# Optimization experiments

Hardware: AMD Instinct MI355X
Metric: run time of the kernel (lower is better)

## Reference

```python
import jax, jax.numpy as jnp
import numpy as np

B, T, D = 2048, 100, 128
HID = [512, 256, 128]
ALPHA, NOISE_STD = 0.2, 0.05


def _lin_init(key, fan_in, fan_out):
    k1, k2 = jax.random.split(key)
    b = 1.0 / np.sqrt(fan_in)
    W = jax.random.uniform(k1, (fan_in, fan_out), minval=-b, maxval=b, dtype=jnp.float32)
    bias = jax.random.uniform(k2, (fan_out,), minval=-b, maxval=b, dtype=jnp.float32)
    return W, bias


def setup_inputs() -> dict:
    key = jax.random.key(0)
    ks = jax.random.split(key, 10)
    x = jax.random.normal(ks[0], (B, T, D), dtype=jnp.float32)
    noise = jax.random.normal(ks[1], (B, T - 1, HID[-1]), dtype=jnp.float32)
    e_w0, e_b0 = _lin_init(ks[2], D, HID[0])
    e_w1, e_b1 = _lin_init(ks[3], HID[0], HID[1])
    e_w2, e_b2 = _lin_init(ks[4], HID[1], HID[2])
    d_w0, d_b0 = _lin_init(ks[5], HID[2], HID[1])
    d_w1, d_b1 = _lin_init(ks[6], HID[1], HID[0])
    d_w2, d_b2 = _lin_init(ks[7], HID[0], D)
    m = jax.random.normal(ks[8], (HID[-1], 2), dtype=jnp.float32)
    n = jax.random.normal(ks[9], (HID[-1], 2), dtype=jnp.float32)
    return {"x": x, "noise": noise, "seq_len": T,
            "e_w0": e_w0, "e_b0": e_b0, "e_w1": e_w1, "e_b1": e_b1,
            "e_w2": e_w2, "e_b2": e_b2, "d_w0": d_w0, "d_b0": d_b0,
            "d_w1": d_w1, "d_b1": d_b1, "d_w2": d_w2, "d_b2": d_b2,
            "m": m, "n": n}


def reference(x, noise, seq_len, e_w0, e_b0, e_w1, e_b1, e_w2, e_b2,
              d_w0, d_b0, d_w1, d_b1, d_w2, d_b2, m, n):
    hs = m.shape[0]  # latent size (128)
    x = jnp.where(jnp.isnan(x), 0.0, x)  # NaN masking as in Autoencoder.forward

    def encoder(v):
        v = jax.nn.relu(v @ e_w0 + e_b0)
        v = jax.nn.relu(v @ e_w1 + e_b1)
        return v @ e_w2 + e_b2

    def decoder(v):
        v = jax.nn.relu(v @ d_w0 + d_b0)
        v = jax.nn.relu(v @ d_w1 + d_b1)
        return v @ d_w2 + d_b2

    h_enc = encoder(x)              # (B, T, hs)
    x_reconstruct = decoder(h_enc)  # (B, T, D)
    h0 = h_enc[:, 0, :]             # (B, hs)
    x0 = x[:, 0, :]                 # (B, D)

    def step(h, nz):
        r = jnp.tanh(h)
        # low-rank recurrence: rank-2 update m n^T / hidden_size
        dh = ALPHA * (-h + (r @ n) @ m.T / hs) + NOISE_STD * nz
        h = h + dh
        out = decoder(jnp.tanh(h))
        return h, (h, out)

    _, (zs, outs) = jax.lax.scan(step, h0, jnp.swapaxes(noise, 0, 1))
    z_pred = jnp.concatenate([h0[:, None, :], jnp.swapaxes(zs, 0, 1)], axis=1)
    x_pred = jnp.concatenate([x0[:, None, :], jnp.swapaxes(outs, 0, 1)], axis=1)
    return x_pred, x_reconstruct, z_pred
```

## Files before the change

kernel.cpp:

```cpp
#include <hip/hip_runtime.h>
#include <math.h>

namespace {

constexpr int B_  = 2048;
constexpr int T_  = 100;
constexpr int D_  = 128;
constexpr int BT_ = B_ * T_;
constexpr int M_  = 64;

using f32x4  = __attribute__((ext_vector_type(4))) float;
using bf16x8 = __attribute__((ext_vector_type(8))) __bf16;

enum { MODE_ENC = 0, MODE_ID = 1, MODE_TANH = 2 };

__device__ __forceinline__ unsigned short f2bf(float f) {
  unsigned int u = __float_as_uint(f);
  return (unsigned short)((u + 0x7FFFu + ((u >> 16) & 1u)) >> 16);
}
__device__ __forceinline__ unsigned int pack2(float a, float b) {
  return (unsigned int)f2bf(a) | ((unsigned int)f2bf(b) << 16);
}
__device__ __forceinline__ float ftanh(float x) {
  const float e = __expf(2.0f * x);
  return 1.0f - 2.0f / (e + 1.0f);
}

template <int KGEMM, int NT, int KFW>
__device__ __forceinline__ void gemm(const char* __restrict__ A, const int astr,
                                     const unsigned short* __restrict__ Wt,
                                     f32x4 (&acc)[NT][4], const int lrow, const int lk) {
  constexpr int NK = KGEMM / 32;
  const int key = lrow << 4;
  const unsigned short* wl = Wt + lk * 8;
#pragma unroll
  for (int kk = 0; kk < NK; ++kk) {
    int4 breg[NT];
#pragma unroll
    for (int nt = 0; nt < NT; ++nt)
      breg[nt] = *reinterpret_cast<const int4*>(
          wl + (size_t)(nt * 16 + lrow) * KFW + kk * 32);
    bf16x8 act[4];
#pragma unroll
    for (int s = 0; s < 4; ++s)
      act[s] = __builtin_bit_cast(bf16x8,
          *reinterpret_cast<const int4*>(A + (s * 16 + lrow) * astr + ((kk * 64 + lk * 16) ^ key)));
#pragma unroll
    for (int nt = 0; nt < NT; ++nt) {
      const bf16x8 w = __builtin_bit_cast(bf16x8, breg[nt]);
#pragma unroll
      for (int s = 0; s < 4; ++s)
        acc[nt][s] = __builtin_amdgcn_mfma_f32_16x16x32_bf16(w, act[s], acc[nt][s], 0, 0, 0);
    }
  }
}

template <int NT>
__device__ __forceinline__ void init_bias(f32x4 (&acc)[NT][4], const float* __restrict__ bias,
                                          const int lk) {
#pragma unroll
  for (int nt = 0; nt < NT; ++nt) {
    const f32x4 bv = *reinterpret_cast<const f32x4*>(bias + nt * 16 + lk * 4);
#pragma unroll
    for (int s = 0; s < 4; ++s) acc[nt][s] = bv;
  }
}

template <int NT, bool RELU>
__device__ __forceinline__ void store_lds_pk(char* __restrict__ dst, const int strideB,
                                             const int colLocal0, f32x4 (&acc)[NT][4],
                                             const int lrow, const int lk) {
  const int key = lrow << 4;
#pragma unroll
  for (int nt = 0; nt < NT; ++nt) {
    const int colb = (colLocal0 + nt * 16 + lk * 4) * 2;
#pragma unroll
    for (int s = 0; s < 4; ++s) {
      float v0 = acc[nt][s][0], v1 = acc[nt][s][1], v2 = acc[nt][s][2], v3 = acc[nt][s][3];
      if (RELU) {
        v0 = fmaxf(v0, 0.f); v1 = fmaxf(v1, 0.f); v2 = fmaxf(v2, 0.f); v3 = fmaxf(v3, 0.f);
      }
      uint2 w;
      w.x = pack2(v0, v1);
      w.y = pack2(v2, v3);
      *reinterpret_cast<uint2*>(dst + (s * 16 + lrow) * strideB + (colb ^ key)) = w;
    }
  }
}

template <int MODE>
__device__ __forceinline__ int rowmap(const int rl) {
  if constexpr (MODE == MODE_TANH) {
    const int b = rl / 99;
    return b * T_ + (rl - b * 99) + 1;
  }
  return rl;
}

template <int MODE>
__device__ __forceinline__ void store_global(float* __restrict__ gout, f32x4 (&acc)[1][4],
                                             const int r0, const int col0,
                                             const int lrow, const int lk) {
#pragma unroll
  for (int s = 0; s < 4; ++s) {
    const int g = rowmap<MODE>(r0 + s * 16 + lrow);
    *reinterpret_cast<float4*>(gout + (size_t)g * D_ + col0 + lk * 4) =
        __builtin_bit_cast(float4, acc[0][s]);
  }
}

template <int MODE>
__device__ __forceinline__ void stage(const float* __restrict__ in, char* __restrict__ X,
                                      float* __restrict__ xpred0,
                                      const int r0, const int tid) {
#pragma unroll
  for (int i = 0; i < 2; ++i) {
    const int c   = tid + i * 512;
    const int row = c >> 4;
    const int cb  = c & 15;
    const int rl  = r0 + row;
    const int g   = rowmap<MODE>(rl);
    const float4* gp = reinterpret_cast<const float4*>(in + (size_t)g * D_ + cb * 8);
    float4 v0 = gp[0], v1 = gp[1];
    if constexpr (MODE == MODE_ENC) {
      v0.x = (v0.x == v0.x) ? v0.x : 0.f;  v0.y = (v0.y == v0.y) ? v0.y : 0.f;
      v0.z = (v0.z == v0.z) ? v0.z : 0.f;  v0.w = (v0.w == v0.w) ? v0.w : 0.f;
      v1.x = (v1.x == v1.x) ? v1.x : 0.f;  v1.y = (v1.y == v1.y) ? v1.y : 0.f;
      v1.z = (v1.z == v1.z) ? v1.z : 0.f;  v1.w = (v1.w == v1.w) ? v1.w : 0.f;
      if (rl % T_ == 0) {
        float4* xp = reinterpret_cast<float4*>(xpred0 + (size_t)g * D_ + cb * 8);
        xp[0] = v0; xp[1] = v1;
      }
    }
    if constexpr (MODE == MODE_TANH) {
      v0.x = ftanh(v0.x); v0.y = ftanh(v0.y); v0.z = ftanh(v0.z); v0.w = ftanh(v0.w);
      v1.x = ftanh(v1.x); v1.y = ftanh(v1.y); v1.z = ftanh(v1.z); v1.w = ftanh(v1.w);
    }
    int4 pk;
    pk.x = (int)pack2(v0.x, v0.y); pk.y = (int)pack2(v0.z, v0.w);
    pk.z = (int)pack2(v1.x, v1.y); pk.w = (int)pack2(v1.z, v1.w);
    *reinterpret_cast<int4*>(X + row * 256 + ((cb * 16) ^ ((row & 15) << 4))) = pk;
  }
}

template <int MODE>
__device__ __forceinline__ void dec_body(const unsigned short* __restrict__ dW0t, const float* __restrict__ d_b0,
                                         const unsigned short* __restrict__ dW1t, const float* __restrict__ d_b1,
                                         const unsigned short* __restrict__ dW2t, const float* __restrict__ d_b2,
                                         float* __restrict__ gout,
                                         char* __restrict__ X, char* __restrict__ Y,
                                         const int r0, const int wave, const int lrow, const int lk) {
  f32x4 acc1[2][4];
  init_bias<2>(acc1, d_b0 + wave * 32, lk);
  gemm<128, 2, 128>(X, 256, dW0t + (size_t)(wave * 32) * 128, acc1, lrow, lk);
  store_lds_pk<2, true>(Y, 512, wave * 32, acc1, lrow, lk);
  __syncthreads();

  f32x4 acc3[1][4];
  init_bias<1>(acc3, d_b2 + wave * 16, lk);
#pragma unroll
  for (int q = 0; q < 4; ++q) {
    f32x4 acc2[1][4];
    init_bias<1>(acc2, d_b1 + q * 128 + wave * 16, lk);
    gemm<256, 1, 256>(Y, 512, dW1t + (size_t)(q * 128 + wave * 16) * 256, acc2, lrow, lk);
    if (q) __syncthreads();
    store_lds_pk<1, true>(X, 256, wave * 16, acc2, lrow, lk);
    __syncthreads();
    gemm<128, 1, 512>(X, 256, dW2t + (size_t)(wave * 16) * 512 + q * 128, acc3, lrow, lk);
  }
  store_global<MODE>(gout, acc3, r0, wave * 16, lrow, lk);
}

__launch_bounds__(512, 4)
__global__ void enc_dec_kernel(const float* __restrict__ in,
                               const unsigned short* __restrict__ eW0t, const float* __restrict__ e_b0,
                               const unsigned short* __restrict__ eW1t, const float* __restrict__ e_b1,
                               const unsigned short* __restrict__ eW2t, const float* __restrict__ e_b2,
                               const unsigned short* __restrict__ dW0t, const float* __restrict__ d_b0,
                               const unsigned short* __restrict__ dW1t, const float* __restrict__ d_b1,
                               const unsigned short* __restrict__ dW2t, const float* __restrict__ d_b2,
                               float* __restrict__ z, float* __restrict__ x_rec,
                               float* __restrict__ x_pred) {
  __shared__ __align__(16) char X[M_ * 256];
  __shared__ __align__(16) char Y[M_ * 512];

  const int tid  = threadIdx.x;
  const int wave = tid >> 6;
  const int lane = tid & 63;
  const int lrow = lane & 15;
  const int lk   = lane >> 4;
  const int r0   = blockIdx.x * M_;

  stage<MODE_ENC>(in, X, x_pred, r0, tid);
  __syncthreads();

  f32x4 acc2[2][4];
  init_bias<2>(acc2, e_b1 + wave * 32, lk);
#pragma unroll
  for (int h = 0; h < 2; ++h) {
    f32x4 acc1[2][4];
    init_bias<2>(acc1, e_b0 + h * 256 + wave * 32, lk);
    gemm<128, 2, 128>(X, 256, eW0t + (size_t)(h * 256 + wave * 32) * 128, acc1, lrow, lk);
    if (h) __syncthreads();
    store_lds_pk<2, true>(Y, 512, wave * 32, acc1, lrow, lk);
    __syncthreads();
    gemm<256, 2, 512>(Y, 512, eW1t + (size_t)(wave * 32) * 512 + h * 256, acc2, lrow, lk);
  }
  __syncthreads();

  f32x4 acc3[1][4];
  init_bias<1>(acc3, e_b2 + wave * 16, lk);
#pragma unroll
  for (int hh = 0; hh < 2; ++hh) {
    if ((wave >> 2) == hh)
      store_lds_pk<2, true>(X, 256, (wave & 3) * 32, acc2, lrow, lk);
    __syncthreads();
    gemm<128, 1, 256>(X, 256, eW2t + (size_t)(wave * 16) * 256 + hh * 128, acc3, lrow, lk);
    __syncthreads();
  }
  store_lds_pk<1, false>(X, 256, wave * 16, acc3, lrow, lk);
  store_global<MODE_ENC>(z, acc3, r0, wave * 16, lrow, lk);
  __syncthreads();

  dec_body<MODE_ID>(dW0t, d_b0, dW1t, d_b1, dW2t, d_b2, x_rec, X, Y, r0, wave, lrow, lk);
}

__launch_bounds__(512, 4)
__global__ void pred_dec_kernel(const float* __restrict__ zin,
                                const unsigned short* __restrict__ dW0t, const float* __restrict__ d_b0,
                                const unsigned short* __restrict__ dW1t, const float* __restrict__ d_b1,
                                const unsigned short* __restrict__ dW2t, const float* __restrict__ d_b2,
                                float* __restrict__ x_pred) {
  __shared__ __align__(16) char X[M_ * 256];
  __shared__ __align__(16) char Y[M_ * 512];

  const int tid  = threadIdx.x;
  const int wave = tid >> 6;
  const int lane = tid & 63;
  const int lrow = lane & 15;
  const int lk   = lane >> 4;
  const int r0   = blockIdx.x * M_;

  stage<MODE_TANH>(zin, X, nullptr, r0, tid);
  __syncthreads();
  dec_body<MODE_TANH>(dW0t, d_b0, dW1t, d_b1, dW2t, d_b2, x_pred, X, Y, r0, wave, lrow, lk);
}

__global__ void wprep_all_kernel(const float* __restrict__ s0, const float* __restrict__ s1,
                                 const float* __restrict__ s2, const float* __restrict__ s3,
                                 const float* __restrict__ s4, const float* __restrict__ s5,
                                 unsigned short* __restrict__ d0, unsigned short* __restrict__ d1,
                                 unsigned short* __restrict__ d2, unsigned short* __restrict__ d3,
                                 unsigned short* __restrict__ d4, unsigned short* __restrict__ d5) {
  const int id = blockIdx.x * blockDim.x + threadIdx.x;
  const float* src; unsigned short* dst; int K, N, l;
  if (id < 65536)       { src = s0; dst = d0; K = 128; N = 512; l = id; }
  else if (id < 196608) { src = s1; dst = d1; K = 512; N = 256; l = id - 65536; }
  else if (id < 229376) { src = s2; dst = d2; K = 256; N = 128; l = id - 196608; }
  else if (id < 262144) { src = s3; dst = d3; K = 128; N = 256; l = id - 229376; }
  else if (id < 393216) { src = s4; dst = d4; K = 256; N = 512; l = id - 262144; }
  else                  { src = s5; dst = d5; K = 512; N = 128; l = id - 393216; }
  const int k = l / N;
  const int n = l - k * N;
  dst[(size_t)n * K + k] = f2bf(src[l]);
}

__global__ void rnn_scan_kernel(const float* __restrict__ noise,
                                const float* __restrict__ m, const float* __restrict__ n,
                                float* __restrict__ z) {
  const int gtid = blockIdx.x * blockDim.x + threadIdx.x;
  const int b = gtid >> 6;
  const int lane = threadIdx.x & 63;
  const int k0 = lane, k1 = lane + 64;

  const float mk00 = m[k0 * 2], mk01 = m[k0 * 2 + 1];
  const float mk10 = m[k1 * 2], mk11 = m[k1 * 2 + 1];
  const float nk00 = n[k0 * 2], nk01 = n[k0 * 2 + 1];
  const float nk10 = n[k1 * 2], nk11 = n[k1 * 2 + 1];

  float* zb = z + (size_t)b * T_ * D_;
  const float* nzb = noise + (size_t)b * (T_ - 1) * D_;
  float h0 = zb[k0];
  float h1 = zb[k1];

#pragma unroll 1
  for (int t = 0; t < T_ - 1; ++t) {
    const float r0v = tanhf(h0);
    const float r1v = tanhf(h1);
    float p0 = r0v * nk00 + r1v * nk10;
    float p1 = r0v * nk01 + r1v * nk11;
#pragma unroll
    for (int off = 32; off > 0; off >>= 1) {
      p0 += __shfl_xor(p0, off);
      p1 += __shfl_xor(p1, off);
    }
    const float v0 = (p0 * mk00 + p1 * mk01) * (1.0f / 128.0f);
    const float v1 = (p0 * mk10 + p1 * mk11) * (1.0f / 128.0f);
    const float nz0 = nzb[t * D_ + k0];
    const float nz1 = nzb[t * D_ + k1];
    h0 += 0.2f * (v0 - h0) + 0.05f * nz0;
    h1 += 0.2f * (v1 - h1) + 0.05f * nz1;
    zb[(t + 1) * D_ + k0] = h0;
    zb[(t + 1) * D_ + k1] = h1;
  }
}

}

extern "C" void kernel_launch(void* const* d_in, const int* in_sizes, int n_in,
                              void* d_out, int out_size, void* d_ws, size_t ws_size,
                              hipStream_t stream) {
  (void)in_sizes; (void)n_in; (void)ws_size; (void)out_size;

  const float* x     = (const float*)d_in[0];
  const float* noise = (const float*)d_in[1];
  const float* e_w0 = (const float*)d_in[3];
  const float* e_b0 = (const float*)d_in[4];
  const float* e_w1 = (const float*)d_in[5];
  const float* e_b1 = (const float*)d_in[6];
  const float* e_w2 = (const float*)d_in[7];
  const float* e_b2 = (const float*)d_in[8];
  const float* d_w0 = (const float*)d_in[9];
  const float* d_b0 = (const float*)d_in[10];
  const float* d_w1 = (const float*)d_in[11];
  const float* d_b1 = (const float*)d_in[12];
  const float* d_w2 = (const float*)d_in[13];
  const float* d_b2 = (const float*)d_in[14];
  const float* m    = (const float*)d_in[15];
  const float* n    = (const float*)d_in[16];

  float* out    = (float*)d_out;
  float* x_pred = out;
  float* x_rec  = out + (size_t)BT_ * D_;
  float* z      = out + 2 * (size_t)BT_ * D_;

  unsigned short* ws = (unsigned short*)d_ws;
  unsigned short* eW0t = ws;
  unsigned short* eW1t = ws + 65536;
  unsigned short* eW2t = ws + 196608;
  unsigned short* dW0t = ws + 229376;
  unsigned short* dW1t = ws + 262144;
  unsigned short* dW2t = ws + 393216;

  wprep_all_kernel<<<458752 / 256, 256, 0, stream>>>(e_w0, e_w1, e_w2, d_w0, d_w1, d_w2,
                                                     eW0t, eW1t, eW2t, dW0t, dW1t, dW2t);

  enc_dec_kernel<<<BT_ / M_, 512, 0, stream>>>(x,
      eW0t, e_b0, eW1t, e_b1, eW2t, e_b2,
      dW0t, d_b0, dW1t, d_b1, dW2t, d_b2,
      z, x_rec, x_pred);

  rnn_scan_kernel<<<B_ / 4, 256, 0, stream>>>(noise, m, n, z);

  pred_dec_kernel<<<(B_ * (T_ - 1)) / M_, 512, 0, stream>>>(z,
      dW0t, d_b0, dW1t, d_b1, dW2t, d_b2, x_pred);
}
```

Baseline: 664.5 us.

## Halve row tile to 32 and use 4-wave blocks with wider per-wave column tiles

```diff
diff --git a/kernel.cpp b/kernel.cpp
--- a/kernel.cpp
+++ b/kernel.cpp
@@ -7,7 +7,7 @@
 constexpr int T_  = 100;
 constexpr int D_  = 128;
 constexpr int BT_ = B_ * T_;
-constexpr int M_  = 64;
+constexpr int M_  = 32;
 
 using f32x4  = __attribute__((ext_vector_type(4))) float;
 using bf16x8 = __attribute__((ext_vector_type(8))) __bf16;
@@ -29,7 +29,7 @@
 template <int KGEMM, int NT, int KFW>
 __device__ __forceinline__ void gemm(const char* __restrict__ A, const int astr,
                                      const unsigned short* __restrict__ Wt,
-                                     f32x4 (&acc)[NT][4], const int lrow, const int lk) {
+                                     f32x4 (&acc)[NT][2], const int lrow, const int lk) {
   constexpr int NK = KGEMM / 32;
   const int key = lrow << 4;
   const unsigned short* wl = Wt + lk * 8;
@@ -40,42 +40,42 @@
     for (int nt = 0; nt < NT; ++nt)
       breg[nt] = *reinterpret_cast<const int4*>(
           wl + (size_t)(nt * 16 + lrow) * KFW + kk * 32);
-    bf16x8 act[4];
-#pragma unroll
-    for (int s = 0; s < 4; ++s)
+    bf16x8 act[2];
+#pragma unroll
+    for (int s = 0; s < 2; ++s)
       act[s] = __builtin_bit_cast(bf16x8,
           *reinterpret_cast<const int4*>(A + (s * 16 + lrow) * astr + ((kk * 64 + lk * 16) ^ key)));
 #pragma unroll
     for (int nt = 0; nt < NT; ++nt) {
       const bf16x8 w = __builtin_bit_cast(bf16x8, breg[nt]);
 #pragma unroll
-      for (int s = 0; s < 4; ++s)
+      for (int s = 0; s < 2; ++s)
         acc[nt][s] = __builtin_amdgcn_mfma_f32_16x16x32_bf16(w, act[s], acc[nt][s], 0, 0, 0);
     }
   }
 }
 
 template <int NT>
-__device__ __forceinline__ void init_bias(f32x4 (&acc)[NT][4], const float* __restrict__ bias,
+__device__ __forceinline__ void init_bias(f32x4 (&acc)[NT][2], const float* __restrict__ bias,
                                           const int lk) {
 #pragma unroll
   for (int nt = 0; nt < NT; ++nt) {
     const f32x4 bv = *reinterpret_cast<const f32x4*>(bias + nt * 16 + lk * 4);
 #pragma unroll
-    for (int s = 0; s < 4; ++s) acc[nt][s] = bv;
+    for (int s = 0; s < 2; ++s) acc[nt][s] = bv;
   }
 }
 
 template <int NT, bool RELU>
 __device__ __forceinline__ void store_lds_pk(char* __restrict__ dst, const int strideB,
-                                             const int colLocal0, f32x4 (&acc)[NT][4],
+                                             const int colLocal0, f32x4 (&acc)[NT][2],
                                              const int lrow, const int lk) {
   const int key = lrow << 4;
 #pragma unroll
   for (int nt = 0; nt < NT; ++nt) {
     const int colb = (colLocal0 + nt * 16 + lk * 4) * 2;
 #pragma unroll
-    for (int s = 0; s < 4; ++s) {
+    for (int s = 0; s < 2; ++s) {
       float v0 = acc[nt][s][0], v1 = acc[nt][s][1], v2 = acc[nt][s][2], v3 = acc[nt][s][3];
       if (RELU) {
         v0 = fmaxf(v0, 0.f); v1 = fmaxf(v1, 0.f); v2 = fmaxf(v2, 0.f); v3 = fmaxf(v3, 0.f);
@@ -97,15 +97,17 @@
   return rl;
 }
 
-template <int MODE>
-__device__ __forceinline__ void store_global(float* __restrict__ gout, f32x4 (&acc)[1][4],
+template <int MODE, int NT>
+__device__ __forceinline__ void store_global(float* __restrict__ gout, f32x4 (&acc)[NT][2],
                                              const int r0, const int col0,
                                              const int lrow, const int lk) {
 #pragma unroll
-  for (int s = 0; s < 4; ++s) {
+  for (int s = 0; s < 2; ++s) {
     const int g = rowmap<MODE>(r0 + s * 16 + lrow);
-    *reinterpret_cast<float4*>(gout + (size_t)g * D_ + col0 + lk * 4) =
-        __builtin_bit_cast(float4, acc[0][s]);
+    float* gr = gout + (size_t)g * D_ + col0 + lk * 4;
+#pragma unroll
+    for (int nt = 0; nt < NT; ++nt)
+      *reinterpret_cast<float4*>(gr + nt * 16) = __builtin_bit_cast(float4, acc[nt][s]);
   }
 }
 
@@ -115,7 +117,7 @@
                                       const int r0, const int tid) {
 #pragma unroll
   for (int i = 0; i < 2; ++i) {
-    const int c   = tid + i * 512;
+    const int c   = tid + i * 256;
     const int row = c >> 4;
     const int cb  = c & 15;
     const int rl  = r0 + row;
@@ -150,28 +152,31 @@
                                          float* __restrict__ gout,
                                          char* __restrict__ X, char* __restrict__ Y,
                                          const int r0, const int wave, const int lrow, const int lk) {
-  f32x4 acc1[2][4];
-  init_bias<2>(acc1, d_b0 + wave * 32, lk);
-  gemm<128, 2, 128>(X, 256, dW0t + (size_t)(wave * 32) * 128, acc1, lrow, lk);
-  store_lds_pk<2, true>(Y, 512, wave * 32, acc1, lrow, lk);
-  __syncthreads();
-
-  f32x4 acc3[1][4];
-  init_bias<1>(acc3, d_b2 + wave * 16, lk);
+#pragma unroll
+  for (int p = 0; p < 2; ++p) {
+    f32x4 acc1[2][2];
+    init_bias<2>(acc1, d_b0 + p * 128 + wave * 32, lk);
+    gemm<128, 2, 128>(X, 256, dW0t + (size_t)(p * 128 + wave * 32) * 128, acc1, lrow, lk);
+    store_lds_pk<2, true>(Y, 512, p * 128 + wave * 32, acc1, lrow, lk);
+  }
+  __syncthreads();
+
+  f32x4 acc3[2][2];
+  init_bias<2>(acc3, d_b2 + wave * 32, lk);
 #pragma unroll
   for (int q = 0; q < 4; ++q) {
-    f32x4 acc2[1][4];
-    init_bias<1>(acc2, d_b1 + q * 128 + wave * 16, lk);
-    gemm<256, 1, 256>(Y, 512, dW1t + (size_t)(q * 128 + wave * 16) * 256, acc2, lrow, lk);
+    f32x4 acc2[2][2];
+    init_bias<2>(acc2, d_b1 + q * 128 + wave * 32, lk);
+    gemm<256, 2, 256>(Y, 512, dW1t + (size_t)(q * 128 + wave * 32) * 256, acc2, lrow, lk);
     if (q) __syncthreads();
-    store_lds_pk<1, true>(X, 256, wave * 16, acc2, lrow, lk);
+    store_lds_pk<2, true>(X, 256, wave * 32, acc2, lrow, lk);
     __syncthreads();
-    gemm<128, 1, 512>(X, 256, dW2t + (size_t)(wave * 16) * 512 + q * 128, acc3, lrow, lk);
-  }
-  store_global<MODE>(gout, acc3, r0, wave * 16, lrow, lk);
-}
-
-__launch_bounds__(512, 4)
+    gemm<128, 2, 512>(X, 256, dW2t + (size_t)(wave * 32) * 512 + q * 128, acc3, lrow, lk);
+  }
+  store_global<MODE, 2>(gout, acc3, r0, wave * 32, lrow, lk);
+}
+
+__launch_bounds__(256, 4)
 __global__ void enc_dec_kernel(const float* __restrict__ in,
                                const unsigned short* __restrict__ eW0t, const float* __restrict__ e_b0,
                                const unsigned short* __restrict__ eW1t, const float* __restrict__ e_b1,
@@ -194,38 +199,44 @@
   stage<MODE_ENC>(in, X, x_pred, r0, tid);
   __syncthreads();
 
-  f32x4 acc2[2][4];
-  init_bias<2>(acc2, e_b1 + wave * 32, lk);
+  f32x4 acc2[2][2][2];
+#pragma unroll
+  for (int p2 = 0; p2 < 2; ++p2)
+    init_bias<2>(acc2[p2], e_b1 + p2 * 128 + wave * 32, lk);
 #pragma unroll
   for (int h = 0; h < 2; ++h) {
-    f32x4 acc1[2][4];
-    init_bias<2>(acc1, e_b0 + h * 256 + wave * 32, lk);
-    gemm<128, 2, 128>(X, 256, eW0t + (size_t)(h * 256 + wave * 32) * 128, acc1, lrow, lk);
     if (h) __syncthreads();
-    store_lds_pk<2, true>(Y, 512, wave * 32, acc1, lrow, lk);
+#pragma unroll
+    for (int p = 0; p < 2; ++p) {
+      f32x4 acc1[2][2];
+      init_bias<2>(acc1, e_b0 + h * 256 + p * 128 + wave * 32, lk);
+      gemm<128, 2, 128>(X, 256, eW0t + (size_t)(h * 256 + p * 128 + wave * 32) * 128, acc1, lrow, lk);
+      store_lds_pk<2, true>(Y, 512, p * 128 + wave * 32, acc1, lrow, lk);
+    }
     __syncthreads();
-    gemm<256, 2, 512>(Y, 512, eW1t + (size_t)(wave * 32) * 512 + h * 256, acc2, lrow, lk);
-  }
-  __syncthreads();
-
-  f32x4 acc3[1][4];
-  init_bias<1>(acc3, e_b2 + wave * 16, lk);
-#pragma unroll
-  for (int hh = 0; hh < 2; ++hh) {
-    if ((wave >> 2) == hh)
-      store_lds_pk<2, true>(X, 256, (wave & 3) * 32, acc2, lrow, lk);
-    __syncthreads();
-    gemm<128, 1, 256>(X, 256, eW2t + (size_t)(wave * 16) * 256 + hh * 128, acc3, lrow, lk);
-    __syncthreads();
-  }
-  store_lds_pk<1, false>(X, 256, wave * 16, acc3, lrow, lk);
-  store_global<MODE_ENC>(z, acc3, r0, wave * 16, lrow, lk);
+#pragma unroll
+    for (int p2 = 0; p2 < 2; ++p2)
+      gemm<256, 2, 512>(Y, 512, eW1t + (size_t)(p2 * 128 + wave * 32) * 512 + h * 256,
+                        acc2[p2], lrow, lk);
+  }
+  __syncthreads();
+
+#pragma unroll
+  for (int p2 = 0; p2 < 2; ++p2)
+    store_lds_pk<2, true>(Y, 512, p2 * 128 + wave * 32, acc2[p2], lrow, lk);
+  __syncthreads();
+
+  f32x4 acc3[2][2];
+  init_bias<2>(acc3, e_b2 + wave * 32, lk);
+  gemm<256, 2, 256>(Y, 512, eW2t + (size_t)(wave * 32) * 256, acc3, lrow, lk);
+  store_lds_pk<2, false>(X, 256, wave * 32, acc3, lrow, lk);
+  store_global<MODE_ENC, 2>(z, acc3, r0, wave * 32, lrow, lk);
   __syncthreads();
 
   dec_body<MODE_ID>(dW0t, d_b0, dW1t, d_b1, dW2t, d_b2, x_rec, X, Y, r0, wave, lrow, lk);
 }
 
-__launch_bounds__(512, 4)
+__launch_bounds__(256, 4)
 __global__ void pred_dec_kernel(const float* __restrict__ zin,
                                 const unsigned short* __restrict__ dW0t, const float* __restrict__ d_b0,
                                 const unsigned short* __restrict__ dW1t, const float* __restrict__ d_b1,
@@ -345,13 +356,13 @@
   wprep_all_kernel<<<458752 / 256, 256, 0, stream>>>(e_w0, e_w1, e_w2, d_w0, d_w1, d_w2,
                                                      eW0t, eW1t, eW2t, dW0t, dW1t, dW2t);
 
-  enc_dec_kernel<<<BT_ / M_, 512, 0, stream>>>(x,
+  enc_dec_kernel<<<BT_ / M_, 256, 0, stream>>>(x,
       eW0t, e_b0, eW1t, e_b1, eW2t, e_b2,
       dW0t, d_b0, dW1t, d_b1, dW2t, d_b2,
       z, x_rec, x_pred);
 
   rnn_scan_kernel<<<B_ / 4, 256, 0, stream>>>(noise, m, n, z);
 
-  pred_dec_kernel<<<(B_ * (T_ - 1)) / M_, 512, 0, stream>>>(z,
+  pred_dec_kernel<<<(B_ * (T_ - 1)) / M_, 256, 0, stream>>>(z,
       dW0t, d_b0, dW1t, d_b1, dW2t, d_b2, x_pred);
 }
```

Result: slower. 1.117 ms (+68.0%).
